# Kernel tuning notes

Hardware: AMD Instinct MI355X
Metric: run time of the kernel (lower is better)

Reference implementation:

```python
import jax, jax.numpy as jnp
import numpy as np

HPC = 42  # HPC_FEATURES_LEN

def setup_inputs() -> dict:
    key = jax.random.key(0)
    ks = jax.random.split(key, 8)
    B, N, C, P, S = 4, 16384, 103, 2048, 32
    xyz = jax.random.normal(ks[0], (B, N, 3), dtype=jnp.float32)
    features = jax.random.normal(ks[1], (B, C, N), dtype=jnp.float32)
    new_xyz = jax.random.normal(ks[2], (B, P, 3), dtype=jnp.float32)
    idx = jax.random.randint(ks[3], (B, P, S), 0, N, dtype=jnp.int32)
    # 1x1-conv weights (out_ch, in_ch); gate conv sees full 3+C=106 channels
    Wg = jax.random.normal(ks[4], (64, 106), dtype=jnp.float32) * 0.05
    bg = jnp.zeros((64,), dtype=jnp.float32)
    W1 = jax.random.normal(ks[5], (64, 64), dtype=jnp.float32) * 0.05
    b1 = jnp.zeros((64,), dtype=jnp.float32)
    W2 = jax.random.normal(ks[6], (128, 64), dtype=jnp.float32) * 0.05
    b2 = jnp.zeros((128,), dtype=jnp.float32)
    W3 = jax.random.normal(ks[7], (256, 128), dtype=jnp.float32) * 0.05
    b3 = jnp.zeros((256,), dtype=jnp.float32)
    return {"xyz": xyz, "features": features, "new_xyz": new_xyz, "idx": idx,
            "Wg": Wg, "bg": bg, "W1": W1, "b1": b1, "W2": W2, "b2": b2,
            "W3": W3, "b3": b3}

def reference(xyz, features, new_xyz, idx, Wg, bg, W1, b1, W2, b2, W3, b3):
    # --- grouping: gather neighbors, center xyz, concat features ---
    # grouped_xyz: (B, P, S, 3) -> (B, 3, P, S)
    grouped_xyz = jax.vmap(lambda x, i: x[i])(xyz, idx) - new_xyz[:, :, None, :]
    grouped_xyz = jnp.transpose(grouped_xyz, (0, 3, 1, 2))
    # grouped_feat: (B, C, P, S)
    grouped_feat = jax.vmap(lambda f, i: f[:, i])(features, idx)
    nf = jnp.concatenate([grouped_xyz, grouped_feat], axis=1)  # (B, 3+C, P, S)
    base = nf[:, :-HPC]                                        # (B, 3+C-42, P, S)
    # --- gating 1x1 conv on full channels, then elementwise gate ---
    w = jnp.einsum('bcps,oc->bops', nf, Wg) + bg[None, :, None, None]
    x = base * (1.0 + w)
    # --- 1x1-conv MLP stack with ReLU ---
    for W, b in ((W1, b1), (W2, b2), (W3, b3)):
        x = jax.nn.relu(jnp.einsum('bcps,oc->bops', x, W) + b[None, :, None, None])
    # --- max pool over nsample ---
    pooled = jnp.max(x, axis=-1)  # (B, 256, P)
    return new_xyz, pooled
```

## Files before the change

### kernel.cpp

```cpp
#include <hip/hip_runtime.h>
#include <stdint.h>


namespace {
constexpr int kB = 4, kN = 16384, kC = 103, kP = 2048, kS = 32;

using short8 = __attribute__((ext_vector_type(8))) short;
using short4 = __attribute__((ext_vector_type(4))) short;
using f32x4  = __attribute__((ext_vector_type(4))) float;

constexpr int WG_HI = 0,     WG_LO = 8192;
constexpr int W1_HI = 16384, W1_LO = 20480;
constexpr int W2_HI = 24576, W2_LO = 32768;
constexpr int W3_HI = 40960, W3_LO = 73728;
constexpr size_t FT_OFF    = 262144;
constexpr size_t FT_SHORTS = (size_t)kB * kN * 128;
constexpr size_t WS_NEED   = FT_OFF + 2 * FT_SHORTS * 2;

__device__ __forceinline__ unsigned short f2bf(float x) {
    unsigned u = __float_as_uint(x);
    u += 0x7fffu + ((u >> 16) & 1u);
    return (unsigned short)(u >> 16);
}
__device__ __forceinline__ float bf2f(unsigned short h) {
    return __uint_as_float((unsigned)h << 16);
}
__device__ __forceinline__ unsigned cvtpk(float a, float b) {
    unsigned r;
    asm("v_cvt_pk_bf16_f32 %0, %1, %2" : "=v"(r) : "v"(a), "v"(b));
    return r;
}
__device__ __forceinline__ void pack4(const float v[4], uint2& H, uint2& L) {
    H.x = cvtpk(v[0], v[1]);
    H.y = cvtpk(v[2], v[3]);
    const float r0 = v[0] - __uint_as_float(H.x << 16);
    const float r1 = v[1] - __uint_as_float(H.x & 0xffff0000u);
    const float r2 = v[2] - __uint_as_float(H.y << 16);
    const float r3 = v[3] - __uint_as_float(H.y & 0xffff0000u);
    L.x = cvtpk(r0, r1);
    L.y = cvtpk(r2, r3);
}
__device__ __forceinline__ f32x4 mfma3(short8 ah, short8 al, short8 bh, short8 bl, f32x4 acc) {
    acc = __builtin_amdgcn_mfma_f32_16x16x32_bf16(ah, bh, acc, 0, 0, 0);
    acc = __builtin_amdgcn_mfma_f32_16x16x32_bf16(ah, bl, acc, 0, 0, 0);
    acc = __builtin_amdgcn_mfma_f32_16x16x32_bf16(al, bh, acc, 0, 0, 0);
    return acc;
}

__global__ void copy_newxyz(const float* __restrict__ src, float* __restrict__ dst, int n) {
    int i = blockIdx.x * blockDim.x + threadIdx.x;
    if (i < n) dst[i] = src[i];
}

__global__ void prep_weights(const float* __restrict__ Wg, const float* __restrict__ W1,
                             const float* __restrict__ W2, const float* __restrict__ W3,
                             short* __restrict__ ws) {
    int i = blockIdx.x * blockDim.x + threadIdx.x;
    if (i >= 53248) return;
    float w; int hi, lo, j;
    if (i < 8192)       { j = i;         int o = j >> 7, c = j & 127; w = (c < 106) ? Wg[o * 106 + c] : 0.f; hi = WG_HI; lo = WG_LO; }
    else if (i < 12288) { j = i - 8192;  int o = j >> 6, c = j & 63;  w = W1[o * 64 + c];  hi = W1_HI; lo = W1_LO; }
    else if (i < 20480) { j = i - 12288; int o = j >> 6, c = j & 63;  w = W2[o * 64 + c];  hi = W2_HI; lo = W2_LO; }
    else                { j = i - 20480; int o = j >> 7, c = j & 127; w = W3[o * 128 + c]; hi = W3_HI; lo = W3_LO; }
    unsigned short h = f2bf(w);
    ws[hi + j] = (short)h;
    ws[lo + j] = (short)f2bf(w - bf2f(h));
}

__global__ __launch_bounds__(512) void prep_feat(const float* __restrict__ f,
                                                 short* __restrict__ ftH, short* __restrict__ ftL) {
    __shared__ float tile[kC][65];
    const int bb = blockIdx.x >> 8;
    const int n0 = (blockIdx.x & 255) * 64;
    const int tid = threadIdx.x;
    for (int c = tid >> 6; c < kC; c += 8)
        tile[c][tid & 63] = f[((size_t)bb * kC + c) * kN + n0 + (tid & 63)];
    __syncthreads();
    const int np = tid >> 3, gc = tid & 7;
    short* rH = ftH + ((size_t)bb * kN + n0 + np) * 128;
    short* rL = ftL + ((size_t)bb * kN + n0 + np) * 128;
    #pragma unroll
    for (int kk = 0; kk < 2; ++kk) {
        const int chunk = gc + 8 * kk;
        union { uint4 u; short s[8]; } H, L;
        #pragma unroll
        for (int e = 0; e < 8; ++e) {
            const int col = chunk * 8 + e;
            float v = (col >= 3 && col < 106) ? tile[col - 3][np] : 0.f;
            unsigned short hh = f2bf(v);
            H.s[e] = (short)hh;
            L.s[e] = (short)f2bf(v - bf2f(hh));
        }
        *(uint4*)(rH + chunk * 8) = H.u;
        *(uint4*)(rL + chunk * 8) = L.u;
    }
}

template<int NOT, int NPT, int KT, int LDC, int LDW, bool INIT>
__device__ __forceinline__ void gemm_core(
    const short* __restrict__ xh, const short* __restrict__ xl,
    const short* __restrict__ wh, const short* __restrict__ wl,
    const float* __restrict__ bias, int kwoff,
    int ot0, int pt0t, int lane, f32x4 (&acc)[NOT][NPT])
{
    const int q = lane >> 4, n16 = lane & 15;
    short8 whr[NOT * KT], wlr[NOT * KT];
    #pragma unroll
    for (int i = 0; i < NOT; ++i)
        #pragma unroll
        for (int kt = 0; kt < KT; ++kt) {
            const size_t we = (size_t)((ot0 + i) * 16 + n16) * LDW + kwoff + kt * 32 + q * 8;
            whr[i * KT + kt] = *(const short8*)(wh + we);
            wlr[i * KT + kt] = *(const short8*)(wl + we);
        }
    if constexpr (INIT) {
        #pragma unroll
        for (int i = 0; i < NOT; ++i) {
            const f32x4 binit = *(const f32x4*)(bias + (ot0 + i) * 16 + 4 * q);
            #pragma unroll
            for (int j = 0; j < NPT; ++j) acc[i][j] = binit;
        }
    }
    __builtin_amdgcn_sched_barrier(0);
    #pragma unroll
    for (int kt = 0; kt < KT; ++kt) {
        const int k0 = kt * 32 + q * 8;
        short8 bh[NPT], bl[NPT];
        #pragma unroll
        for (int j = 0; j < NPT; ++j) {
            const int p = (pt0t + j) * 16 + n16;
            const int e = p * LDC + (k0 ^ ((p & 7) << 3));
            bh[j] = *(const short8*)(xh + e);
            bl[j] = *(const short8*)(xl + e);
        }
        #pragma unroll
        for (int i = 0; i < NOT; ++i) {
            const short8 ah = whr[i * KT + kt];
            const short8 al = wlr[i * KT + kt];
            #pragma unroll
            for (int j = 0; j < NPT; ++j) acc[i][j] = mfma3(ah, al, bh[j], bl[j], acc[i][j]);
        }
    }
}

template<int NOT, int NPT, bool GATE, int LDCO>
__device__ __forceinline__ void store_act(
    f32x4 (&acc)[NOT][NPT], short* __restrict__ oh, short* __restrict__ ol,
    const short* __restrict__ nfh, const short* __restrict__ nfl,
    int ot0, int pt0t, int lane)
{
    const int q = lane >> 4, n16 = lane & 15;
    #pragma unroll
    for (int i = 0; i < NOT; ++i) {
        const int ob = (ot0 + i) * 16 + 4 * q;
        #pragma unroll
        for (int j = 0; j < NPT; ++j) {
            const int p = (pt0t + j) * 16 + n16;
            const int cs = ob ^ ((p & 7) << 3);
            float v[4];
            if (GATE) {
                const short4 h4 = *(const short4*)(nfh + p * 128 + cs);
                const short4 l4 = *(const short4*)(nfl + p * 128 + cs);
                #pragma unroll
                for (int r = 0; r < 4; ++r) {
                    const float base = bf2f((unsigned short)h4[r]) + bf2f((unsigned short)l4[r]);
                    v[r] = fmaf(base, acc[i][j][r], base);
                }
            } else {
                #pragma unroll
                for (int r = 0; r < 4; ++r) v[r] = fmaxf(acc[i][j][r], 0.f);
            }
            uint2 H, L;
            pack4(v, H, L);
            *(uint2*)(oh + p * LDCO + cs) = H;
            *(uint2*)(ol + p * LDCO + cs) = L;
        }
    }
}

template<bool DENSE>
__global__ __launch_bounds__(512, 2) void pointnet_sa(
    const float* __restrict__ xyz, const float* __restrict__ features,
    const float* __restrict__ new_xyz, const int* __restrict__ idx,
    const short* __restrict__ ws, const short* __restrict__ ftH, const short* __restrict__ ftL,
    const float* __restrict__ bg, const float* __restrict__ b1,
    const float* __restrict__ b2, const float* __restrict__ b3,
    float* __restrict__ out_pooled)
{
    __shared__ alignas(16) short smem[24576];
    short* NFh = smem;
    short* NFl = smem + 8192;
    short* X0h = smem + 16384;
    short* X0l = smem + 20480;

    const int tid = threadIdx.x, lane = tid & 63, wave = tid >> 6;
    const int q = lane >> 4, n16 = lane & 15;
    const int pt0 = blockIdx.x * 64;
    const int b = pt0 >> 16;

    if (DENSE) {
        const int gp = tid >> 3, gc = tid & 7;
        const int pt = pt0 + gp;
        const int n = idx[pt];
        const short* rH = ftH + ((size_t)b * kN + n) * 128;
        const short* rL = ftL + ((size_t)b * kN + n) * 128;
        uint4 hc0 = *(const uint4*)(rH + gc * 8);
        uint4 hc1 = *(const uint4*)(rH + gc * 8 + 64);
        uint4 lc0 = *(const uint4*)(rL + gc * 8);
        uint4 lc1 = *(const uint4*)(rL + gc * 8 + 64);
        if (gc == 0) {
            const float* xp = xyz + ((size_t)b * kN + n) * 3;
            const int pp = (pt >> 5) & (kP - 1);
            const float* np = new_xyz + ((size_t)b * kP + pp) * 3;
            union { uint4 u; short s[8]; } H, L;
            H.u = hc0; L.u = lc0;
            #pragma unroll
            for (int c = 0; c < 3; ++c) {
                const float v = xp[c] - np[c];
                const unsigned short hh = f2bf(v);
                H.s[c] = (short)hh;
                L.s[c] = (short)f2bf(v - bf2f(hh));
            }
            hc0 = H.u; lc0 = L.u;
        }
        const int sw = (gc ^ (gp & 7)) * 8;
        *(uint4*)(NFh + gp * 128 + sw)      = hc0;
        *(uint4*)(NFh + gp * 128 + sw + 64) = hc1;
        *(uint4*)(NFl + gp * 128 + sw)      = lc0;
        *(uint4*)(NFl + gp * 128 + sw + 64) = lc1;
    } else {
        const int p = tid & 63;
        const int cg = tid >> 6;
        const int pt = pt0 + p;
        const int n = idx[pt];
        const int pp = (pt >> 5) & (kP - 1);
        const float* fbp = features + (size_t)b * kC * kN + n;
        const float* xp = xyz + ((size_t)b * kN + n) * 3;
        const float* np = new_xyz + ((size_t)b * kP + pp) * 3;
        for (int c = cg; c < 128; c += 8) {
            float v;
            if (c < 3)        v = xp[c] - np[c];
            else if (c < 106) v = fbp[(size_t)(c - 3) * kN];
            else              v = 0.f;
            const unsigned short h = f2bf(v);
            const int cs = c ^ ((p & 7) << 3);
            NFh[p * 128 + cs] = (short)h;
            NFl[p * 128 + cs] = (short)f2bf(v - bf2f(h));
        }
    }
    __syncthreads();

    {
        f32x4 a[1][2];
        gemm_core<1, 2, 4, 128, 128, true>(NFh, NFl, ws + WG_HI, ws + WG_LO, bg, 0,
                                           wave & 3, 2 * (wave >> 2), lane, a);
        store_act<1, 2, true, 64>(a, X0h, X0l, NFh, NFl, wave & 3, 2 * (wave >> 2), lane);
    }
    __syncthreads();

    {
        f32x4 a[1][2];
        gemm_core<1, 2, 2, 64, 64, true>(X0h, X0l, ws + W1_HI, ws + W1_LO, b1, 0,
                                         wave & 3, 2 * (wave >> 2), lane, a);
        store_act<1, 2, false, 128>(a, NFh, NFl, nullptr, nullptr,
                                    wave & 3, 2 * (wave >> 2), lane);
    }
    __syncthreads();

    {
        f32x4 a[2][2];
        gemm_core<2, 2, 2, 128, 64, true>(NFh, NFl, ws + W2_HI, ws + W2_LO, b2, 0,
                                          2 * (wave & 3), 2 * (wave >> 2), lane, a);
        if ((wave & 3) < 2)
            store_act<2, 2, false, 64>(a, X0h, X0l, nullptr, nullptr,
                                       2 * (wave & 3), 2 * (wave >> 2), lane);
        else
            store_act<2, 2, false, 128>(a, NFh + 64, NFl + 64, nullptr, nullptr,
                                        (2 * (wave & 3)) & 3, 2 * (wave >> 2), lane);
    }
    __syncthreads();

    {
        f32x4 a[2][4];
        gemm_core<2, 4, 2, 64, 128, true >(X0h, X0l, ws + W3_HI, ws + W3_LO, b3, 0,
                                           2 * wave, 0, lane, a);
        gemm_core<2, 4, 2, 128, 128, false>(NFh + 64, NFl + 64, ws + W3_HI, ws + W3_LO,
                                            nullptr, 64, 2 * wave, 0, lane, a);
        #pragma unroll
        for (int i = 0; i < 2; ++i) {
            #pragma unroll
            for (int sg = 0; sg < 2; ++sg) {
                #pragma unroll
                for (int r = 0; r < 4; ++r) {
                    float v = fmaxf(a[i][2 * sg][r], a[i][2 * sg + 1][r]);
                    v = fmaxf(v, __shfl_xor(v, 1, 16));
                    v = fmaxf(v, __shfl_xor(v, 2, 16));
                    v = fmaxf(v, __shfl_xor(v, 4, 16));
                    v = fmaxf(v, __shfl_xor(v, 8, 16));
                    v = fmaxf(v, 0.f);
                    if (n16 == 0) {
                        const int o = (2 * wave + i) * 16 + 4 * q + r;
                        const int g = (pt0 >> 5) + sg;
                        out_pooled[((size_t)(g >> 11) * 256 + o) * kP + (g & (kP - 1))] = v;
                    }
                }
            }
        }
    }
}
}

extern "C" void kernel_launch(void* const* d_in, const int* in_sizes, int n_in,
                              void* d_out, int out_size, void* d_ws, size_t ws_size,
                              hipStream_t stream) {
    const float* xyz      = (const float*)d_in[0];
    const float* features = (const float*)d_in[1];
    const float* new_xyz  = (const float*)d_in[2];
    const int*   idx      = (const int*)d_in[3];
    const float* Wg = (const float*)d_in[4];
    const float* bg = (const float*)d_in[5];
    const float* W1 = (const float*)d_in[6];
    const float* b1 = (const float*)d_in[7];
    const float* W2 = (const float*)d_in[8];
    const float* b2 = (const float*)d_in[9];
    const float* W3 = (const float*)d_in[10];
    const float* b3 = (const float*)d_in[11];
    float* out = (float*)d_out;
    short* ws  = (short*)d_ws;
    short* ftH = (short*)((char*)d_ws + FT_OFF);
    short* ftL = ftH + FT_SHORTS;

    const int nxyz = kB * kP * 3;
    copy_newxyz<<<(nxyz + 255) / 256, 256, 0, stream>>>(new_xyz, out, nxyz);
    prep_weights<<<(53248 + 255) / 256, 256, 0, stream>>>(Wg, W1, W2, W3, ws);

    float* pooled = out + nxyz;
    if (ws_size >= WS_NEED) {
        prep_feat<<<kB * (kN / 64), 512, 0, stream>>>(features, ftH, ftL);
        pointnet_sa<true><<<(kB * kP * kS) / 64, 512, 0, stream>>>(
            xyz, features, new_xyz, idx, ws, ftH, ftL, bg, b1, b2, b3, pooled);
    } else {
        pointnet_sa<false><<<(kB * kP * kS) / 64, 512, 0, stream>>>(
            xyz, features, new_xyz, idx, ws, nullptr, nullptr, bg, b1, b2, b3, pooled);
    }
}
```

Measured before the change: 190.5 us.

## Halve block to 4 waves with larger per-wave tiles and inline weight loads

Shrinks the fused PointNet block from 8 to 4 waves per 64-point tile. Each wave now computes twice as many output tiles in every layer: full 64 points in the gate/W1/W2 stages and 4 output tiles in W3. The grouping gather is redistributed over fewer threads. Weight fragments are now loaded inside the k-loop instead of being preloaded into registers behind a sched_barrier, trading register pressure for more global/L1 weight traffic. Launch bounds change to (256,3) to favour more resident blocks, with the risk of less latency hiding per block.

After: 207.6 us. +9.0%, slower.

```diff
diff --git a/kernel.cpp b/kernel.cpp
--- a/kernel.cpp
+++ b/kernel.cpp
@@ -104,15 +104,6 @@
     int ot0, int pt0t, int lane, f32x4 (&acc)[NOT][NPT])
 {
     const int q = lane >> 4, n16 = lane & 15;
-    short8 whr[NOT * KT], wlr[NOT * KT];
-    #pragma unroll
-    for (int i = 0; i < NOT; ++i)
-        #pragma unroll
-        for (int kt = 0; kt < KT; ++kt) {
-            const size_t we = (size_t)((ot0 + i) * 16 + n16) * LDW + kwoff + kt * 32 + q * 8;
-            whr[i * KT + kt] = *(const short8*)(wh + we);
-            wlr[i * KT + kt] = *(const short8*)(wl + we);
-        }
     if constexpr (INIT) {
         #pragma unroll
         for (int i = 0; i < NOT; ++i) {
@@ -121,7 +112,6 @@
             for (int j = 0; j < NPT; ++j) acc[i][j] = binit;
         }
     }
-    __builtin_amdgcn_sched_barrier(0);
     #pragma unroll
     for (int kt = 0; kt < KT; ++kt) {
         const int k0 = kt * 32 + q * 8;
@@ -135,8 +125,9 @@
         }
         #pragma unroll
         for (int i = 0; i < NOT; ++i) {
-            const short8 ah = whr[i * KT + kt];
-            const short8 al = wlr[i * KT + kt];
+            const size_t we = (size_t)((ot0 + i) * 16 + n16) * LDW + kwoff + k0;
+            const short8 ah = *(const short8*)(wh + we);
+            const short8 al = *(const short8*)(wl + we);
             #pragma unroll
             for (int j = 0; j < NPT; ++j) acc[i][j] = mfma3(ah, al, bh[j], bl[j], acc[i][j]);
         }
@@ -179,7 +170,7 @@
 }
 
 template<bool DENSE>
-__global__ __launch_bounds__(512, 2) void pointnet_sa(
+__global__ __launch_bounds__(256, 3) void pointnet_sa(
     const float* __restrict__ xyz, const float* __restrict__ features,
     const float* __restrict__ new_xyz, const int* __restrict__ idx,
     const short* __restrict__ ws, const short* __restrict__ ftH, const short* __restrict__ ftL,
@@ -199,21 +190,23 @@
     const int b = pt0 >> 16;
 
     if (DENSE) {
-        const int gp = tid >> 3, gc = tid & 7;
+        const int gp = tid >> 2, gc = tid & 3;
         const int pt = pt0 + gp;
         const int n = idx[pt];
         const short* rH = ftH + ((size_t)b * kN + n) * 128;
         const short* rL = ftL + ((size_t)b * kN + n) * 128;
-        uint4 hc0 = *(const uint4*)(rH + gc * 8);
-        uint4 hc1 = *(const uint4*)(rH + gc * 8 + 64);
-        uint4 lc0 = *(const uint4*)(rL + gc * 8);
-        uint4 lc1 = *(const uint4*)(rL + gc * 8 + 64);
+        uint4 h[4], l[4];
+        #pragma unroll
+        for (int k = 0; k < 4; ++k) {
+            h[k] = *(const uint4*)(rH + (gc + 4 * k) * 8);
+            l[k] = *(const uint4*)(rL + (gc + 4 * k) * 8);
+        }
         if (gc == 0) {
             const float* xp = xyz + ((size_t)b * kN + n) * 3;
             const int pp = (pt >> 5) & (kP - 1);
             const float* np = new_xyz + ((size_t)b * kP + pp) * 3;
             union { uint4 u; short s[8]; } H, L;
-            H.u = hc0; L.u = lc0;
+            H.u = h[0]; L.u = l[0];
             #pragma unroll
             for (int c = 0; c < 3; ++c) {
                 const float v = xp[c] - np[c];
@@ -221,13 +214,14 @@
                 H.s[c] = (short)hh;
                 L.s[c] = (short)f2bf(v - bf2f(hh));
             }
-            hc0 = H.u; lc0 = L.u;
-        }
-        const int sw = (gc ^ (gp & 7)) * 8;
-        *(uint4*)(NFh + gp * 128 + sw)      = hc0;
-        *(uint4*)(NFh + gp * 128 + sw + 64) = hc1;
-        *(uint4*)(NFl + gp * 128 + sw)      = lc0;
-        *(uint4*)(NFl + gp * 128 + sw + 64) = lc1;
+            h[0] = H.u; l[0] = L.u;
+        }
+        #pragma unroll
+        for (int k = 0; k < 4; ++k) {
+            const int sw = ((gc + 4 * k) ^ (gp & 7)) * 8;
+            *(uint4*)(NFh + gp * 128 + sw) = h[k];
+            *(uint4*)(NFl + gp * 128 + sw) = l[k];
+        }
     } else {
         const int p = tid & 63;
         const int cg = tid >> 6;
@@ -237,7 +231,7 @@
         const float* fbp = features + (size_t)b * kC * kN + n;
         const float* xp = xyz + ((size_t)b * kN + n) * 3;
         const float* np = new_xyz + ((size_t)b * kP + pp) * 3;
-        for (int c = cg; c < 128; c += 8) {
+        for (int c = cg; c < 128; c += 4) {
             float v;
             if (c < 3)        v = xp[c] - np[c];
             else if (c < 106) v = fbp[(size_t)(c - 3) * kN];
@@ -251,43 +245,41 @@
     __syncthreads();
 
     {
-        f32x4 a[1][2];
-        gemm_core<1, 2, 4, 128, 128, true>(NFh, NFl, ws + WG_HI, ws + WG_LO, bg, 0,
-                                           wave & 3, 2 * (wave >> 2), lane, a);
-        store_act<1, 2, true, 64>(a, X0h, X0l, NFh, NFl, wave & 3, 2 * (wave >> 2), lane);
+        f32x4 a[1][4];
+        gemm_core<1, 4, 4, 128, 128, true>(NFh, NFl, ws + WG_HI, ws + WG_LO, bg, 0,
+                                           wave, 0, lane, a);
+        store_act<1, 4, true, 64>(a, X0h, X0l, NFh, NFl, wave, 0, lane);
     }
     __syncthreads();
 
     {
-        f32x4 a[1][2];
-        gemm_core<1, 2, 2, 64, 64, true>(X0h, X0l, ws + W1_HI, ws + W1_LO, b1, 0,
-                                         wave & 3, 2 * (wave >> 2), lane, a);
-        store_act<1, 2, false, 128>(a, NFh, NFl, nullptr, nullptr,
-                                    wave & 3, 2 * (wave >> 2), lane);
-    }
-    __syncthreads();
-
-    {
-        f32x4 a[2][2];
-        gemm_core<2, 2, 2, 128, 64, true>(NFh, NFl, ws + W2_HI, ws + W2_LO, b2, 0,
-                                          2 * (wave & 3), 2 * (wave >> 2), lane, a);
-        if ((wave & 3) < 2)
-            store_act<2, 2, false, 64>(a, X0h, X0l, nullptr, nullptr,
-                                       2 * (wave & 3), 2 * (wave >> 2), lane);
-        else
-            store_act<2, 2, false, 128>(a, NFh + 64, NFl + 64, nullptr, nullptr,
-                                        (2 * (wave & 3)) & 3, 2 * (wave >> 2), lane);
+        f32x4 a[1][4];
+        gemm_core<1, 4, 2, 64, 64, true>(X0h, X0l, ws + W1_HI, ws + W1_LO, b1, 0,
+                                         wave, 0, lane, a);
+        store_act<1, 4, false, 128>(a, NFh, NFl, nullptr, nullptr, wave, 0, lane);
     }
     __syncthreads();
 
     {
         f32x4 a[2][4];
-        gemm_core<2, 4, 2, 64, 128, true >(X0h, X0l, ws + W3_HI, ws + W3_LO, b3, 0,
-                                           2 * wave, 0, lane, a);
-        gemm_core<2, 4, 2, 128, 128, false>(NFh + 64, NFl + 64, ws + W3_HI, ws + W3_LO,
-                                            nullptr, 64, 2 * wave, 0, lane, a);
-        #pragma unroll
-        for (int i = 0; i < 2; ++i) {
+        gemm_core<2, 4, 2, 128, 64, true>(NFh, NFl, ws + W2_HI, ws + W2_LO, b2, 0,
+                                          2 * wave, 0, lane, a);
+        if (wave < 2)
+            store_act<2, 4, false, 64>(a, X0h, X0l, nullptr, nullptr, 2 * wave, 0, lane);
+        else
+            store_act<2, 4, false, 128>(a, NFh + 64, NFl + 64, nullptr, nullptr,
+                                        2 * wave - 4, 0, lane);
+    }
+    __syncthreads();
+
+    {
+        f32x4 a[4][4];
+        gemm_core<4, 4, 2, 64, 128, true >(X0h, X0l, ws + W3_HI, ws + W3_LO, b3, 0,
+                                           4 * wave, 0, lane, a);
+        gemm_core<4, 4, 2, 128, 128, false>(NFh + 64, NFl + 64, ws + W3_HI, ws + W3_LO,
+                                            nullptr, 64, 4 * wave, 0, lane, a);
+        #pragma unroll
+        for (int i = 0; i < 4; ++i) {
             #pragma unroll
             for (int sg = 0; sg < 2; ++sg) {
                 #pragma unroll
@@ -299,7 +291,7 @@
                     v = fmaxf(v, __shfl_xor(v, 8, 16));
                     v = fmaxf(v, 0.f);
                     if (n16 == 0) {
-                        const int o = (2 * wave + i) * 16 + 4 * q + r;
+                        const int o = (4 * wave + i) * 16 + 4 * q + r;
                         const int g = (pt0 >> 5) + sg;
                         out_pooled[((size_t)(g >> 11) * 256 + o) * kP + (g & (kP - 1))] = v;
                     }
@@ -337,10 +329,10 @@
     float* pooled = out + nxyz;
     if (ws_size >= WS_NEED) {
         prep_feat<<<kB * (kN / 64), 512, 0, stream>>>(features, ftH, ftL);
-        pointnet_sa<true><<<(kB * kP * kS) / 64, 512, 0, stream>>>(
+        pointnet_sa<true><<<(kB * kP * kS) / 64, 256, 0, stream>>>(
             xyz, features, new_xyz, idx, ws, ftH, ftL, bg, b1, b2, b3, pooled);
     } else {
-        pointnet_sa<false><<<(kB * kP * kS) / 64, 512, 0, stream>>>(
+        pointnet_sa<false><<<(kB * kP * kS) / 64, 256, 0, stream>>>(
             xyz, features, new_xyz, idx, ws, nullptr, nullptr, bg, b1, b2, b3, pooled);
     }
 }
```

## Gather neighbor rows directly into LDS and stream weight loads inside the k loop

Applied to the files above, without the earlier changes.

The dense gather path now uses global_load_lds to copy the pre-split bf16 hi/lo feature rows straight into shared memory with the same XOR swizzle, skipping the register round trip. The centered xyz values are then patched into LDS after a vmcnt wait. Separately, the GEMM core no longer preloads all weight fragments into registers ahead of the k loop and drops the sched barrier. Weights are instead loaded per k-step, which lowers register pressure but may expose load latency.

Result: faster. 183.0 us, median of 3 (-3.9%).

```diff
diff --git a/kernel.cpp b/kernel.cpp
--- a/kernel.cpp
+++ b/kernel.cpp
@@ -1,6 +1,9 @@
 #include <hip/hip_runtime.h>
 #include <stdint.h>
 
+
+#define AS1 __attribute__((address_space(1)))
+#define AS3 __attribute__((address_space(3)))
 
 namespace {
 constexpr int kB = 4, kN = 16384, kC = 103, kP = 2048, kS = 32;
@@ -45,6 +48,9 @@
     acc = __builtin_amdgcn_mfma_f32_16x16x32_bf16(ah, bl, acc, 0, 0, 0);
     acc = __builtin_amdgcn_mfma_f32_16x16x32_bf16(al, bh, acc, 0, 0, 0);
     return acc;
+}
+__device__ __forceinline__ void glds16(const short* g, short* l) {
+    __builtin_amdgcn_global_load_lds((const AS1 unsigned int*)g, (AS3 unsigned int*)l, 16, 0, 0);
 }
 
 __global__ void copy_newxyz(const float* __restrict__ src, float* __restrict__ dst, int n) {
@@ -104,15 +110,6 @@
     int ot0, int pt0t, int lane, f32x4 (&acc)[NOT][NPT])
 {
     const int q = lane >> 4, n16 = lane & 15;
-    short8 whr[NOT * KT], wlr[NOT * KT];
-    #pragma unroll
-    for (int i = 0; i < NOT; ++i)
-        #pragma unroll
-        for (int kt = 0; kt < KT; ++kt) {
-            const size_t we = (size_t)((ot0 + i) * 16 + n16) * LDW + kwoff + kt * 32 + q * 8;
-            whr[i * KT + kt] = *(const short8*)(wh + we);
-            wlr[i * KT + kt] = *(const short8*)(wl + we);
-        }
     if constexpr (INIT) {
         #pragma unroll
         for (int i = 0; i < NOT; ++i) {
@@ -121,7 +118,6 @@
             for (int j = 0; j < NPT; ++j) acc[i][j] = binit;
         }
     }
-    __builtin_amdgcn_sched_barrier(0);
     #pragma unroll
     for (int kt = 0; kt < KT; ++kt) {
         const int k0 = kt * 32 + q * 8;
@@ -135,8 +131,9 @@
         }
         #pragma unroll
         for (int i = 0; i < NOT; ++i) {
-            const short8 ah = whr[i * KT + kt];
-            const short8 al = wlr[i * KT + kt];
+            const size_t we = (size_t)((ot0 + i) * 16 + n16) * LDW + kwoff + k0;
+            const short8 ah = *(const short8*)(wh + we);
+            const short8 al = *(const short8*)(wl + we);
             #pragma unroll
             for (int j = 0; j < NPT; ++j) acc[i][j] = mfma3(ah, al, bh[j], bl[j], acc[i][j]);
         }
@@ -199,35 +196,39 @@
     const int b = pt0 >> 16;
 
     if (DENSE) {
-        const int gp = tid >> 3, gc = tid & 7;
-        const int pt = pt0 + gp;
-        const int n = idx[pt];
-        const short* rH = ftH + ((size_t)b * kN + n) * 128;
-        const short* rL = ftL + ((size_t)b * kN + n) * 128;
-        uint4 hc0 = *(const uint4*)(rH + gc * 8);
-        uint4 hc1 = *(const uint4*)(rH + gc * 8 + 64);
-        uint4 lc0 = *(const uint4*)(rL + gc * 8);
-        uint4 lc1 = *(const uint4*)(rL + gc * 8 + 64);
-        if (gc == 0) {
+        const int l16 = lane >> 4;
+        const int c16 = lane & 15;
+        #pragma unroll
+        for (int cg = 0; cg < 2; ++cg) {
+            const int gp = wave * 8 + cg * 4 + l16;
+            const int pt = pt0 + gp;
+            const int n = idx[pt];
+            const size_t row = ((size_t)b * kN + n) * 128;
+            const int sc = (c16 ^ (gp & 7)) * 8;
+            const int lbase = __builtin_amdgcn_readfirstlane((wave * 8 + cg * 4) * 128);
+            glds16(ftH + row + sc, smem + lbase);
+            glds16(ftL + row + sc, smem + 8192 + lbase);
+        }
+        float xd0 = 0.f, xd1 = 0.f, xd2 = 0.f;
+        if ((lane & 7) == 0) {
+            const int gp = wave * 8 + (lane >> 3);
+            const int pt = pt0 + gp;
+            const int n = idx[pt];
             const float* xp = xyz + ((size_t)b * kN + n) * 3;
             const int pp = (pt >> 5) & (kP - 1);
             const float* np = new_xyz + ((size_t)b * kP + pp) * 3;
-            union { uint4 u; short s[8]; } H, L;
-            H.u = hc0; L.u = lc0;
-            #pragma unroll
-            for (int c = 0; c < 3; ++c) {
-                const float v = xp[c] - np[c];
-                const unsigned short hh = f2bf(v);
-                H.s[c] = (short)hh;
-                L.s[c] = (short)f2bf(v - bf2f(hh));
-            }
-            hc0 = H.u; lc0 = L.u;
-        }
-        const int sw = (gc ^ (gp & 7)) * 8;
-        *(uint4*)(NFh + gp * 128 + sw)      = hc0;
-        *(uint4*)(NFh + gp * 128 + sw + 64) = hc1;
-        *(uint4*)(NFl + gp * 128 + sw)      = lc0;
-        *(uint4*)(NFl + gp * 128 + sw + 64) = lc1;
+            xd0 = xp[0] - np[0]; xd1 = xp[1] - np[1]; xd2 = xp[2] - np[2];
+        }
+        asm volatile("s_waitcnt vmcnt(0)" ::: "memory");
+        if ((lane & 7) == 0) {
+            const int gp = wave * 8 + (lane >> 3);
+            const int o = gp * 128 + (gp & 7) * 8;
+            const unsigned short h0 = f2bf(xd0), h1 = f2bf(xd1), h2 = f2bf(xd2);
+            NFh[o + 0] = (short)h0; NFh[o + 1] = (short)h1; NFh[o + 2] = (short)h2;
+            NFl[o + 0] = (short)f2bf(xd0 - bf2f(h0));
+            NFl[o + 1] = (short)f2bf(xd1 - bf2f(h1));
+            NFl[o + 2] = (short)f2bf(xd2 - bf2f(h2));
+        }
     } else {
         const int p = tid & 63;
         const int cg = tid >> 6;
```
